# Kernel optimization log

Hardware: AMD Instinct MI355X
Metric: run time of the kernel (lower is better)

Reference implementation:

```python
import jax, jax.numpy as jnp
import numpy as np
import math

B, N, D, H, DK, DI, L, C = 4, 512, 1024, 16, 64, 4096, 6, 16000
EPS = 1e-5


def pe_table(n, d):
    # faithful to PE() with d_inp == d_model == d
    pos = jnp.arange(n, dtype=jnp.float32)[:, None]
    div = jnp.exp(jnp.arange(0, d, 2, dtype=jnp.float32) * (-math.log(10000.0) / d))
    p = jnp.zeros((n, d), jnp.float32)
    p = p.at[:, 0::2].set(jnp.sin(pos * div))
    p = p.at[:, 1::2].set(jnp.cos(pos * div))
    return p[None]  # [1, n, d] broadcasts over batch (== torch repeat)


def layer_norm(x, g, b):
    mu = jnp.mean(x, -1, keepdims=True)
    var = jnp.mean(jnp.square(x - mu), -1, keepdims=True)
    return (x - mu) / jnp.sqrt(var + EPS) * g + b


def mha(q_in, k_in, v_in, Wq, Wk, Wv, Wo, mask):
    # Wq/Wk/Wv: [H, D, DK]; batched equivalent of the per-head Linear loop
    q = jnp.einsum('bnd,hdk->bhnk', q_in, Wq)
    k = jnp.einsum('bmd,hdk->bhmk', k_in, Wk)
    v = jnp.einsum('bmd,hdk->bhmk', v_in, Wv)
    s = jnp.einsum('bhnk,bhmk->bhnm', q, k) / math.sqrt(q.shape[-1])
    s = jnp.where(mask[:, None] == 0, -jnp.inf, s)
    a = jax.nn.softmax(s, -1)
    o = jnp.einsum('bhnm,bhmk->bhnk', a, v)
    b_, h, n, dv = o.shape
    # concat heads in order (dim=-1) then Wo
    return o.transpose(0, 2, 1, 3).reshape(b_, n, h * dv) @ Wo


def ffn(x, W1, b1, W2, b2):
    return jax.nn.relu(x @ W1 + b1) @ W2 + b2


def transformer_fwd(encoder_input, decoder_input, encoder_mask, decoder_mask,
                    enc_Wq, enc_Wk, enc_Wv, enc_Wo, enc_W1, enc_b1, enc_W2, enc_b2,
                    enc_g1, enc_beta1, enc_g2, enc_beta2,
                    dec_sWq, dec_sWk, dec_sWv, dec_sWo, dec_cWq, dec_cWk, dec_cWv, dec_cWo,
                    dec_W1, dec_b1, dec_W2, dec_b2,
                    dec_g1, dec_beta1, dec_g2, dec_beta2, dec_g3, dec_beta3,
                    pred_W, pred_b):
    n, d = encoder_input.shape[1], encoder_input.shape[2]
    pe = pe_table(n, d)

    def enc_step(x, p):
        Wq, Wk, Wv, Wo, W1, b1, W2, b2, g1, bb1, g2, bb2 = p
        h1 = layer_norm(x + mha(x, x, x, Wq, Wk, Wv, Wo, encoder_mask), g1, bb1)
        return layer_norm(h1 + ffn(h1, W1, b1, W2, b2), g2, bb2), None

    enc_out, _ = jax.lax.scan(
        enc_step, encoder_input + pe,
        (enc_Wq, enc_Wk, enc_Wv, enc_Wo, enc_W1, enc_b1, enc_W2, enc_b2,
         enc_g1, enc_beta1, enc_g2, enc_beta2))

    # decoder uses encoder_mask[:, :t, :] with t == n (full mask here)
    def dec_step(x, p):
        (sWq, sWk, sWv, sWo, cWq, cWk, cWv, cWo,
         W1, b1, W2, b2, g1, bb1, g2, bb2, g3, bb3) = p
        h1 = layer_norm(x + mha(x, x, x, sWq, sWk, sWv, sWo, decoder_mask), g1, bb1)
        h2 = layer_norm(h1 + mha(h1, enc_out, enc_out, cWq, cWk, cWv, cWo, encoder_mask), g2, bb2)
        return layer_norm(h2 + ffn(h2, W1, b1, W2, b2), g3, bb3), None

    dec_out, _ = jax.lax.scan(
        dec_step, decoder_input + pe,
        (dec_sWq, dec_sWk, dec_sWv, dec_sWo, dec_cWq, dec_cWk, dec_cWv, dec_cWo,
         dec_W1, dec_b1, dec_W2, dec_b2,
         dec_g1, dec_beta1, dec_g2, dec_beta2, dec_g3, dec_beta3))

    return jax.nn.softmax(dec_out @ pred_W + pred_b, -1)


def setup_inputs():
    key = jax.random.key(0)
    ks = iter(jax.random.split(key, 32))
    w = lambda *s: jax.random.normal(next(ks), s, jnp.float32) * 0.02
    return {
        'encoder_input': jax.random.normal(next(ks), (B, N, D), jnp.float32),
        'decoder_input': jax.random.normal(next(ks), (B, N, D), jnp.float32),
        'encoder_mask': jnp.ones((B, N, N), jnp.int32),
        'decoder_mask': jnp.tril(jnp.ones((B, N, N), jnp.int32)),  # causal, as Mask()
        'enc_Wq': w(L, H, D, DK), 'enc_Wk': w(L, H, D, DK), 'enc_Wv': w(L, H, D, DK),
        'enc_Wo': w(L, H * DK, D),
        'enc_W1': w(L, D, DI), 'enc_b1': jnp.zeros((L, DI), jnp.float32),
        'enc_W2': w(L, DI, D), 'enc_b2': jnp.zeros((L, D), jnp.float32),
        'enc_g1': jnp.ones((L, D), jnp.float32), 'enc_beta1': jnp.zeros((L, D), jnp.float32),
        'enc_g2': jnp.ones((L, D), jnp.float32), 'enc_beta2': jnp.zeros((L, D), jnp.float32),
        'dec_sWq': w(L, H, D, DK), 'dec_sWk': w(L, H, D, DK), 'dec_sWv': w(L, H, D, DK),
        'dec_sWo': w(L, H * DK, D),
        'dec_cWq': w(L, H, D, DK), 'dec_cWk': w(L, H, D, DK), 'dec_cWv': w(L, H, D, DK),
        'dec_cWo': w(L, H * DK, D),
        'dec_W1': w(L, D, DI), 'dec_b1': jnp.zeros((L, DI), jnp.float32),
        'dec_W2': w(L, DI, D), 'dec_b2': jnp.zeros((L, D), jnp.float32),
        'dec_g1': jnp.ones((L, D), jnp.float32), 'dec_beta1': jnp.zeros((L, D), jnp.float32),
        'dec_g2': jnp.ones((L, D), jnp.float32), 'dec_beta2': jnp.zeros((L, D), jnp.float32),
        'dec_g3': jnp.ones((L, D), jnp.float32), 'dec_beta3': jnp.zeros((L, D), jnp.float32),
        'pred_W': w(D, C), 'pred_b': jnp.zeros((C,), jnp.float32),
    }


def reference(encoder_input, decoder_input, encoder_mask, decoder_mask,
              enc_Wq, enc_Wk, enc_Wv, enc_Wo, enc_W1, enc_b1, enc_W2, enc_b2,
              enc_g1, enc_beta1, enc_g2, enc_beta2,
              dec_sWq, dec_sWk, dec_sWv, dec_sWo, dec_cWq, dec_cWk, dec_cWv, dec_cWo,
              dec_W1, dec_b1, dec_W2, dec_b2,
              dec_g1, dec_beta1, dec_g2, dec_beta2, dec_g3, dec_beta3,
              pred_W, pred_b):
    return transformer_fwd(encoder_input, decoder_input, encoder_mask, decoder_mask,
                           enc_Wq, enc_Wk, enc_Wv, enc_Wo, enc_W1, enc_b1, enc_W2, enc_b2,
                           enc_g1, enc_beta1, enc_g2, enc_beta2,
                           dec_sWq, dec_sWk, dec_sWv, dec_sWo, dec_cWq, dec_cWk, dec_cWv, dec_cWo,
                           dec_W1, dec_b1, dec_W2, dec_b2,
                           dec_g1, dec_beta1, dec_g2, dec_beta2, dec_g3, dec_beta3,
                           pred_W, pred_b)
```

## Files before the change

kernel.cpp:

```cpp
#include <hip/hip_runtime.h>
#include <hip/hip_bf16.h>
#include <cstdint>

using bf16 = __hip_bfloat16;
typedef __attribute__((ext_vector_type(8))) short short8;
typedef __attribute__((ext_vector_type(4))) float floatx4;

constexpr int B_ = 4, N_ = 512, D_ = 1024, H_ = 16, DK_ = 64, DI_ = 4096, L_ = 6, C_ = 16000;
constexpr int M_ = B_ * N_;
constexpr int HK_ = H_ * DK_;

#define GLL16(gp, lp)                                                                         \
    __builtin_amdgcn_global_load_lds((const __attribute__((address_space(1))) void*)(gp),     \
                                     (__attribute__((address_space(3))) void*)(lp), 16, 0, 0)

template<int OUTB, int BIAS, int RELU>
__global__ __launch_bounds__(256)
void gemm_bt(const bf16* __restrict__ Ag, const bf16* __restrict__ Bg,
             void* __restrict__ Cg, const float* __restrict__ bias,
             int Mdim, int Ndim, int Kdim, int lda, int ldb, int ldc,
             int nbH, int gm, long sAb, long sAh, long sBb, long sBh, long sCb, long sCh)
{
    __shared__ bf16 As[128 * 32];
    __shared__ bf16 Bs[128 * 32];

    const int gx = gridDim.x, gy = gridDim.y;
    const int Sz = gx * gy;
    const int nwg = Sz * (int)gridDim.z;
    const int lin = ((int)blockIdx.z * gy + (int)blockIdx.y) * gx + (int)blockIdx.x;
    const int xcd = lin & 7, idx = lin >> 3;
    const int q = nwg >> 3, r = nwg & 7;
    const int w = (xcd < r ? xcd * (q + 1) : r * (q + 1) + (xcd - r) * q) + idx;
    const int bz = w / Sz;
    const int u = w - bz * Sz;
    const int gw = gm * gx;
    const int grp = u / gw;
    const int rem = u - grp * gw;
    const int gm0 = grp * gm;
    const int gsz = min(gm, gy - gm0);
    const int mt = gm0 + rem % gsz;
    const int nt = rem / gsz;
    const int m0 = mt * 128;
    const int n0 = nt * 128;

    const int bb = bz / nbH;
    const int hh = bz - bb * nbH;
    Ag += (long)bb * sAb + (long)hh * sAh;
    Bg += (long)bb * sBb + (long)hh * sBh;
    const long coff = (long)bb * sCb + (long)hh * sCh;

    const int t = threadIdx.x;
    const int lane = t & 63;
    const int wid = t >> 6;
    const int wm = wid & 1, wn = wid >> 1;

    const int sRow = t >> 2;
    const int sColE = (t & 3) * 8;
    const int ar0 = min(m0 + sRow, Mdim - 1);
    const int ar1 = min(m0 + 64 + sRow, Mdim - 1);
    const int br0 = min(n0 + sRow, Ndim - 1);
    const int br1 = min(n0 + 64 + sRow, Ndim - 1);
    const bf16* pa0 = Ag + (long)ar0 * lda + sColE;
    const bf16* pa1 = Ag + (long)ar1 * lda + sColE;
    const bf16* pb0 = Bg + (long)br0 * ldb + sColE;
    const bf16* pb1 = Bg + (long)br1 * ldb + sColE;
    bf16* la0 = As + sRow * 32 + sColE;
    bf16* la1 = As + (64 + sRow) * 32 + sColE;
    bf16* lb0 = Bs + sRow * 32 + sColE;
    bf16* lb1 = Bs + (64 + sRow) * 32 + sColE;

    floatx4 acc[4][4] = {};
    const int fm = lane & 15;
    const int fk = (lane >> 4) * 8;

    for (int k0 = 0; k0 < Kdim; k0 += 32) {
        __syncthreads();
        GLL16(pa0 + k0, la0);
        GLL16(pa1 + k0, la1);
        GLL16(pb0 + k0, lb0);
        GLL16(pb1 + k0, lb1);
        __syncthreads();

        short8 af[4], bfr[4];
        #pragma unroll
        for (int i = 0; i < 4; ++i)
            af[i] = *(const short8*)(As + (wm * 64 + i * 16 + fm) * 32 + fk);
        #pragma unroll
        for (int j = 0; j < 4; ++j)
            bfr[j] = *(const short8*)(Bs + (wn * 64 + j * 16 + fm) * 32 + fk);
        #pragma unroll
        for (int i = 0; i < 4; ++i)
            #pragma unroll
            for (int j = 0; j < 4; ++j)
                acc[i][j] = __builtin_amdgcn_mfma_f32_16x16x32_bf16(af[i], bfr[j], acc[i][j], 0, 0, 0);
    }

    const int rb = (lane >> 4) * 4;
    #pragma unroll
    for (int j = 0; j < 4; ++j) {
        int c = n0 + wn * 64 + j * 16 + fm;
        if (c >= Ndim) continue;
        float bv = BIAS ? bias[c] : 0.f;
        #pragma unroll
        for (int i = 0; i < 4; ++i) {
            #pragma unroll
            for (int r2 = 0; r2 < 4; ++r2) {
                int row = m0 + wm * 64 + i * 16 + rb + r2;
                if (row >= Mdim) continue;
                float v = acc[i][j][r2] + bv;
                if (RELU) v = fmaxf(v, 0.f);
                long cidx = coff + (long)row * ldc + c;
                if (OUTB) ((bf16*)Cg)[cidx] = __float2bfloat16(v);
                else      ((float*)Cg)[cidx] = v;
            }
        }
    }
}

__global__ __launch_bounds__(256)
void transpose_cvt(const float* __restrict__ src, bf16* __restrict__ dst,
                   int Zi, int R, int C,
                   long sSrcZo, long sSrcZi, long sDstZo, long sDstZi, int dstLD)
{
    __shared__ float tile[32][33];
    const int z = blockIdx.z;
    const int zo = z / Zi, zi = z - zo * Zi;
    const float* s = src + (long)zo * sSrcZo + (long)zi * sSrcZi;
    bf16* d = dst + (long)zo * sDstZo + (long)zi * sDstZi;
    const int c0 = blockIdx.x * 32, r0 = blockIdx.y * 32;
    const int tx = threadIdx.x, ty = threadIdx.y;
    #pragma unroll
    for (int k = 0; k < 4; ++k)
        tile[ty + 8 * k][tx] = s[(long)(r0 + ty + 8 * k) * C + (c0 + tx)];
    __syncthreads();
    #pragma unroll
    for (int k = 0; k < 4; ++k) {
        int cc = ty + 8 * k;
        d[(long)(c0 + cc) * dstLD + (r0 + tx)] = __float2bfloat16(tile[tx][cc]);
    }
}

__device__ __forceinline__ float wave_max(float v) {
    #pragma unroll
    for (int o = 32; o > 0; o >>= 1) v = fmaxf(v, __shfl_down(v, o, 64));
    return v;
}
__device__ __forceinline__ float wave_sum(float v) {
    #pragma unroll
    for (int o = 32; o > 0; o >>= 1) v += __shfl_down(v, o, 64);
    return v;
}

__global__ __launch_bounds__(256)
void add_pe(const float* __restrict__ in, float* __restrict__ outf, bf16* __restrict__ outb)
{
    const long i = (long)blockIdx.x * 256 + threadIdx.x;
    const int d = (int)(i & (D_ - 1));
    const int n = (int)((i >> 10) & (N_ - 1));
    const float div = __expf((float)(d & ~1) * (-9.2103403719761836f / (float)D_));
    const float ang = (float)n * div;
    const float pe = (d & 1) ? cosf(ang) : sinf(ang);
    const float v = in[i] + pe;
    outf[i] = v;
    outb[i] = __float2bfloat16(v);
}

template<int CAUSAL>
__global__ __launch_bounds__(256)
void attn_softmax(const float* __restrict__ S, bf16* __restrict__ P)
{
    const int row = blockIdx.x, bh = blockIdx.y;
    const long base = ((long)bh * N_ + row) * N_;
    const int t = threadIdx.x, lane = t & 63, w = t >> 6;
    const int valid = CAUSAL ? row + 1 : N_;
    float v0 = (t < valid) ? S[base + t] * 0.125f : -__builtin_inff();
    float v1 = (t + 256 < valid) ? S[base + t + 256] * 0.125f : -__builtin_inff();
    __shared__ float r1[4], r2[4];
    float m = wave_max(fmaxf(v0, v1));
    if (lane == 0) r1[w] = m;
    __syncthreads();
    const float mx = fmaxf(fmaxf(r1[0], r1[1]), fmaxf(r1[2], r1[3]));
    const float e0 = __expf(v0 - mx);
    const float e1 = __expf(v1 - mx);
    float s = wave_sum(e0 + e1);
    if (lane == 0) r2[w] = s;
    __syncthreads();
    const float inv = 1.f / ((r2[0] + r2[1]) + (r2[2] + r2[3]));
    P[base + t] = __float2bfloat16(e0 * inv);
    P[base + t + 256] = __float2bfloat16(e1 * inv);
}

struct bf16x4 { bf16 a, b, c, d; };

__global__ __launch_bounds__(256)
void add_ln(const float* __restrict__ X, const float* __restrict__ Y,
            const float* __restrict__ g, const float* __restrict__ be,
            float* __restrict__ outf, bf16* __restrict__ outb)
{
    const int row = blockIdx.x;
    const long base = (long)row * D_;
    const int t = threadIdx.x, lane = t & 63, w = t >> 6;
    const float4 xv = ((const float4*)(X + base))[t];
    const float4 yv = ((const float4*)(Y + base))[t];
    const float a0 = xv.x + yv.x, a1 = xv.y + yv.y, a2 = xv.z + yv.z, a3 = xv.w + yv.w;
    float s = a0 + a1 + a2 + a3;
    float qq = a0 * a0 + a1 * a1 + a2 * a2 + a3 * a3;
    #pragma unroll
    for (int o = 32; o > 0; o >>= 1) { s += __shfl_down(s, o, 64); qq += __shfl_down(qq, o, 64); }
    __shared__ float rs[4], rq[4];
    if (lane == 0) { rs[w] = s; rq[w] = qq; }
    __syncthreads();
    const float S = (rs[0] + rs[1]) + (rs[2] + rs[3]);
    const float Q = (rq[0] + rq[1]) + (rq[2] + rq[3]);
    const float mu = S * (1.f / (float)D_);
    const float var = Q * (1.f / (float)D_) - mu * mu;
    const float rstd = rsqrtf(var + 1e-5f);
    const float4 gv = ((const float4*)g)[t];
    const float4 bv = ((const float4*)be)[t];
    const float o0 = (a0 - mu) * rstd * gv.x + bv.x;
    const float o1 = (a1 - mu) * rstd * gv.y + bv.y;
    const float o2 = (a2 - mu) * rstd * gv.z + bv.z;
    const float o3 = (a3 - mu) * rstd * gv.w + bv.w;
    ((float4*)(outf + base))[t] = make_float4(o0, o1, o2, o3);
    bf16x4 pk{__float2bfloat16(o0), __float2bfloat16(o1), __float2bfloat16(o2), __float2bfloat16(o3)};
    ((bf16x4*)(outb + base))[t] = pk;
}

__global__ __launch_bounds__(256)
void softmax_C(float* __restrict__ X)
{
    constexpr int NI = 63;
    const int row = blockIdx.x;
    float* x = X + (long)row * C_;
    const int t = threadIdx.x, lane = t & 63, w = t >> 6;
    float v[NI];
    float m = -__builtin_inff();
    #pragma unroll
    for (int i = 0; i < NI; ++i) {
        int c = t + i * 256;
        v[i] = (c < C_) ? x[c] : -__builtin_inff();
        m = fmaxf(m, v[i]);
    }
    __shared__ float r1[4], r2[4];
    m = wave_max(m);
    if (lane == 0) r1[w] = m;
    __syncthreads();
    const float mx = fmaxf(fmaxf(r1[0], r1[1]), fmaxf(r1[2], r1[3]));
    float s = 0.f;
    #pragma unroll
    for (int i = 0; i < NI; ++i) { v[i] = __expf(v[i] - mx); s += v[i]; }
    s = wave_sum(s);
    if (lane == 0) r2[w] = s;
    __syncthreads();
    const float inv = 1.f / ((r2[0] + r2[1]) + (r2[2] + r2[3]));
    #pragma unroll
    for (int i = 0; i < NI; ++i) {
        int c = t + i * 256;
        if (c < C_) x[c] = v[i] * inv;
    }
}

static inline int cdiv(int a, int b) { return (a + b - 1) / b; }

static void launch_gemm(hipStream_t st, int outb, int bias_en, int relu,
                        const bf16* A, const bf16* Bm, void* C, const float* bias,
                        int M, int N, int K, int lda, int ldb, int ldc,
                        int nbB = 1, int nbH = 1,
                        long sAb = 0, long sAh = 0, long sBb = 0, long sBh = 0,
                        long sCb = 0, long sCh = 0)
{
    const int gmx = cdiv(N, 128), gmy = cdiv(M, 128);
    const int nwg = gmx * gmy * nbB * nbH;
    const int per = nwg > 8 ? nwg / 8 : 1;
    int gm = 1;
    while (gm * gm < per && gm < gmy) ++gm;
    dim3 g(gmx, gmy, nbB * nbH);
    dim3 b(256);
    if (outb) {
        if (relu) gemm_bt<1,1,1><<<g,b,0,st>>>(A,Bm,C,bias,M,N,K,lda,ldb,ldc,nbH,gm,sAb,sAh,sBb,sBh,sCb,sCh);
        else      gemm_bt<1,0,0><<<g,b,0,st>>>(A,Bm,C,bias,M,N,K,lda,ldb,ldc,nbH,gm,sAb,sAh,sBb,sBh,sCb,sCh);
    } else {
        if (bias_en) gemm_bt<0,1,0><<<g,b,0,st>>>(A,Bm,C,bias,M,N,K,lda,ldb,ldc,nbH,gm,sAb,sAh,sBb,sBh,sCb,sCh);
        else         gemm_bt<0,0,0><<<g,b,0,st>>>(A,Bm,C,bias,M,N,K,lda,ldb,ldc,nbH,gm,sAb,sAh,sBb,sBh,sCb,sCh);
    }
}

extern "C" void kernel_launch(void* const* d_in, const int* in_sizes, int n_in,
                              void* d_out, int out_size, void* d_ws, size_t ws_size,
                              hipStream_t stream)
{
    (void)in_sizes; (void)n_in; (void)out_size; (void)ws_size;

    const float* enc_in  = (const float*)d_in[0];
    const float* dec_in  = (const float*)d_in[1];
    const float* enc_Wq  = (const float*)d_in[4];
    const float* enc_Wk  = (const float*)d_in[5];
    const float* enc_Wv  = (const float*)d_in[6];
    const float* enc_Wo  = (const float*)d_in[7];
    const float* enc_W1  = (const float*)d_in[8];
    const float* enc_b1  = (const float*)d_in[9];
    const float* enc_W2  = (const float*)d_in[10];
    const float* enc_b2  = (const float*)d_in[11];
    const float* enc_g1  = (const float*)d_in[12];
    const float* enc_be1 = (const float*)d_in[13];
    const float* enc_g2  = (const float*)d_in[14];
    const float* enc_be2 = (const float*)d_in[15];
    const float* dec_sWq = (const float*)d_in[16];
    const float* dec_sWk = (const float*)d_in[17];
    const float* dec_sWv = (const float*)d_in[18];
    const float* dec_sWo = (const float*)d_in[19];
    const float* dec_cWq = (const float*)d_in[20];
    const float* dec_cWk = (const float*)d_in[21];
    const float* dec_cWv = (const float*)d_in[22];
    const float* dec_cWo = (const float*)d_in[23];
    const float* dec_W1  = (const float*)d_in[24];
    const float* dec_b1  = (const float*)d_in[25];
    const float* dec_W2  = (const float*)d_in[26];
    const float* dec_b2  = (const float*)d_in[27];
    const float* dec_g1  = (const float*)d_in[28];
    const float* dec_be1 = (const float*)d_in[29];
    const float* dec_g2  = (const float*)d_in[30];
    const float* dec_be2 = (const float*)d_in[31];
    const float* dec_g3  = (const float*)d_in[32];
    const float* dec_be3 = (const float*)d_in[33];
    const float* pred_W  = (const float*)d_in[34];
    const float* pred_b  = (const float*)d_in[35];

    char* wsb = (char*)d_ws;
    size_t off = 0;
    auto alloc = [&](size_t bytes) -> void* {
        void* p = wsb + off;
        off += (bytes + 255) & ~(size_t)255;
        return p;
    };

    bf16* encWqkT  = (bf16*)alloc((size_t)L_ * 2 * HK_ * D_ * 2);
    bf16* encWvT   = (bf16*)alloc((size_t)L_ * HK_ * D_ * 2);
    bf16* encWoT   = (bf16*)alloc((size_t)L_ * D_ * HK_ * 2);
    bf16* encW1T   = (bf16*)alloc((size_t)L_ * DI_ * D_ * 2);
    bf16* encW2T   = (bf16*)alloc((size_t)L_ * D_ * DI_ * 2);
    bf16* decSWqkT = (bf16*)alloc((size_t)L_ * 2 * HK_ * D_ * 2);
    bf16* decSWvT  = (bf16*)alloc((size_t)L_ * HK_ * D_ * 2);
    bf16* decSWoT  = (bf16*)alloc((size_t)L_ * D_ * HK_ * 2);
    bf16* decCWqkT = (bf16*)alloc((size_t)L_ * 2 * HK_ * D_ * 2);
    bf16* decCWvT  = (bf16*)alloc((size_t)L_ * HK_ * D_ * 2);
    bf16* decCWoT  = (bf16*)alloc((size_t)L_ * D_ * HK_ * 2);
    bf16* decW1T   = (bf16*)alloc((size_t)L_ * DI_ * D_ * 2);
    bf16* decW2T   = (bf16*)alloc((size_t)L_ * D_ * DI_ * 2);
    bf16* predWT   = (bf16*)alloc((size_t)C_ * D_ * 2);
    float* xf   = (float*)alloc((size_t)M_ * D_ * 4);
    bf16*  xb   = (bf16*) alloc((size_t)M_ * D_ * 2);
    float* dxf  = (float*)alloc((size_t)M_ * D_ * 4);
    bf16*  dxb  = (bf16*) alloc((size_t)M_ * D_ * 2);
    float* h1f  = (float*)alloc((size_t)M_ * D_ * 4);
    bf16*  h1b  = (bf16*) alloc((size_t)M_ * D_ * 2);
    float* h2f  = (float*)alloc((size_t)M_ * D_ * 4);
    bf16*  h2b  = (bf16*) alloc((size_t)M_ * D_ * 2);
    float* tmpf = (float*)alloc((size_t)M_ * D_ * 4);
    bf16*  qkb  = (bf16*) alloc((size_t)M_ * 2 * HK_ * 2);
    bf16*  vtb  = (bf16*) alloc((size_t)HK_ * M_ * 2);
    float* Sb   = (float*)alloc((size_t)B_ * H_ * N_ * N_ * 4);
    bf16*  Pb   = (bf16*) alloc((size_t)B_ * H_ * N_ * N_ * 2);
    bf16*  ob   = (bf16*) alloc((size_t)M_ * HK_ * 2);
    bf16*  hg   = (bf16*) alloc((size_t)M_ * DI_ * 2);

    auto tr = [&](const float* src, bf16* dst, int Zo, int Zi, int R, int C,
                  long sSrcZo, long sSrcZi, long sDstZo, long sDstZi, int dstLD) {
        dim3 g(C / 32, R / 32, Zo * Zi);
        dim3 b(32, 8);
        transpose_cvt<<<g, b, 0, stream>>>(src, dst, Zi, R, C, sSrcZo, sSrcZi, sDstZo, sDstZi, dstLD);
    };
    const long sA_src_o = (long)H_ * D_ * DK_, sA_src_i = (long)D_ * DK_;
    const long sA_dst_i = (long)DK_ * D_;
    tr(enc_Wq,  encWqkT,                     L_, H_, D_, DK_, sA_src_o, sA_src_i, (long)2*HK_*D_, sA_dst_i, D_);
    tr(enc_Wk,  encWqkT + (size_t)HK_*D_,    L_, H_, D_, DK_, sA_src_o, sA_src_i, (long)2*HK_*D_, sA_dst_i, D_);
    tr(enc_Wv,  encWvT,                      L_, H_, D_, DK_, sA_src_o, sA_src_i, (long)HK_*D_,   sA_dst_i, D_);
    tr(enc_Wo,  encWoT,  L_, 1, HK_, D_,  (long)HK_*D_, 0, (long)D_*HK_, 0, HK_);
    tr(enc_W1,  encW1T,  L_, 1, D_, DI_,  (long)D_*DI_, 0, (long)DI_*D_, 0, D_);
    tr(enc_W2,  encW2T,  L_, 1, DI_, D_,  (long)DI_*D_, 0, (long)D_*DI_, 0, DI_);
    tr(dec_sWq, decSWqkT,                    L_, H_, D_, DK_, sA_src_o, sA_src_i, (long)2*HK_*D_, sA_dst_i, D_);
    tr(dec_sWk, decSWqkT + (size_t)HK_*D_,   L_, H_, D_, DK_, sA_src_o, sA_src_i, (long)2*HK_*D_, sA_dst_i, D_);
    tr(dec_sWv, decSWvT,                     L_, H_, D_, DK_, sA_src_o, sA_src_i, (long)HK_*D_,   sA_dst_i, D_);
    tr(dec_sWo, decSWoT, L_, 1, HK_, D_,  (long)HK_*D_, 0, (long)D_*HK_, 0, HK_);
    tr(dec_cWq, decCWqkT,                    L_, H_, D_, DK_, sA_src_o, sA_src_i, (long)2*HK_*D_, sA_dst_i, D_);
    tr(dec_cWk, decCWqkT + (size_t)HK_*D_,   L_, H_, D_, DK_, sA_src_o, sA_src_i, (long)2*HK_*D_, sA_dst_i, D_);
    tr(dec_cWv, decCWvT,                     L_, H_, D_, DK_, sA_src_o, sA_src_i, (long)HK_*D_,   sA_dst_i, D_);
    tr(dec_cWo, decCWoT, L_, 1, HK_, D_,  (long)HK_*D_, 0, (long)D_*HK_, 0, HK_);
    tr(dec_W1,  decW1T,  L_, 1, D_, DI_,  (long)D_*DI_, 0, (long)DI_*D_, 0, D_);
    tr(dec_W2,  decW2T,  L_, 1, DI_, D_,  (long)DI_*D_, 0, (long)D_*DI_, 0, DI_);
    tr(pred_W,  predWT,  1,  1, D_, C_,   0, 0, 0, 0, D_);

    add_pe<<<(M_ * D_) / 256, 256, 0, stream>>>(enc_in, xf, xb);
    add_pe<<<(M_ * D_) / 256, 256, 0, stream>>>(dec_in, dxf, dxb);

    auto attention = [&](const bf16* qin, const bf16* kvin,
                         const bf16* wqk, const bf16* wv, const bf16* wo, bool causal) {
        if (qin == kvin) {
            launch_gemm(stream, 1,0,0, qin, wqk, qkb, nullptr, M_, 2*HK_, D_, D_, D_, 2*HK_);
        } else {
            launch_gemm(stream, 1,0,0, qin,  wqk,                  qkb,       nullptr, M_, HK_, D_, D_, D_, 2*HK_);
            launch_gemm(stream, 1,0,0, kvin, wqk + (size_t)HK_*D_, qkb + HK_, nullptr, M_, HK_, D_, D_, D_, 2*HK_);
        }
        launch_gemm(stream, 1,0,0, wv, kvin, vtb, nullptr, HK_, M_, D_, D_, D_, M_);
        launch_gemm(stream, 0,0,0, qkb, qkb + HK_, Sb, nullptr,
                    N_, N_, DK_, 2*HK_, 2*HK_, N_,
                    B_, H_,
                    (long)N_*2*HK_, (long)DK_,
                    (long)N_*2*HK_, (long)DK_,
                    (long)H_*N_*N_, (long)N_*N_);
        dim3 sg(N_, B_ * H_);
        if (causal) attn_softmax<1><<<sg, 256, 0, stream>>>(Sb, Pb);
        else        attn_softmax<0><<<sg, 256, 0, stream>>>(Sb, Pb);
        launch_gemm(stream, 1,0,0, Pb, vtb, ob, nullptr,
                    N_, DK_, N_, N_, M_, HK_,
                    B_, H_,
                    (long)H_*N_*N_, (long)N_*N_,
                    (long)N_,       (long)DK_*M_,
                    (long)N_*HK_,   (long)DK_);
        launch_gemm(stream, 0,0,0, ob, wo, tmpf, nullptr, M_, D_, HK_, HK_, HK_, D_);
    };

    for (int l = 0; l < L_; ++l) {
        const bf16* wqk = encWqkT + (size_t)l * 2 * HK_ * D_;
        const bf16* wv  = encWvT  + (size_t)l * HK_ * D_;
        const bf16* wo  = encWoT  + (size_t)l * D_ * HK_;
        const bf16* w1  = encW1T  + (size_t)l * DI_ * D_;
        const bf16* w2  = encW2T  + (size_t)l * D_ * DI_;
        attention(xb, xb, wqk, wv, wo, false);
        add_ln<<<M_, 256, 0, stream>>>(xf, tmpf, enc_g1 + l*D_, enc_be1 + l*D_, h1f, h1b);
        launch_gemm(stream, 1,1,1, h1b, w1, hg, enc_b1 + l*DI_, M_, DI_, D_, D_, D_, DI_);
        launch_gemm(stream, 0,1,0, hg, w2, tmpf, enc_b2 + l*D_, M_, D_, DI_, DI_, DI_, D_);
        add_ln<<<M_, 256, 0, stream>>>(h1f, tmpf, enc_g2 + l*D_, enc_be2 + l*D_, xf, xb);
    }

    for (int l = 0; l < L_; ++l) {
        const bf16* swqk = decSWqkT + (size_t)l * 2 * HK_ * D_;
        const bf16* swv  = decSWvT  + (size_t)l * HK_ * D_;
        const bf16* swo  = decSWoT  + (size_t)l * D_ * HK_;
        const bf16* cwqk = decCWqkT + (size_t)l * 2 * HK_ * D_;
        const bf16* cwv  = decCWvT  + (size_t)l * HK_ * D_;
        const bf16* cwo  = decCWoT  + (size_t)l * D_ * HK_;
        const bf16* w1   = decW1T   + (size_t)l * DI_ * D_;
        const bf16* w2   = decW2T   + (size_t)l * D_ * DI_;
        attention(dxb, dxb, swqk, swv, swo, true);
        add_ln<<<M_, 256, 0, stream>>>(dxf, tmpf, dec_g1 + l*D_, dec_be1 + l*D_, h1f, h1b);
        attention(h1b, xb, cwqk, cwv, cwo, false);
        add_ln<<<M_, 256, 0, stream>>>(h1f, tmpf, dec_g2 + l*D_, dec_be2 + l*D_, h2f, h2b);
        launch_gemm(stream, 1,1,1, h2b, w1, hg, dec_b1 + l*DI_, M_, DI_, D_, D_, D_, DI_);
        launch_gemm(stream, 0,1,0, hg, w2, tmpf, dec_b2 + l*D_, M_, D_, DI_, DI_, DI_, D_);
        add_ln<<<M_, 256, 0, stream>>>(h2f, tmpf, dec_g3 + l*D_, dec_be3 + l*D_, dxf, dxb);
    }

    launch_gemm(stream, 0,1,0, dxb, predWT, d_out, pred_b, M_, C_, D_, D_, D_, C_);
    softmax_C<<<M_, 256, 0, stream>>>((float*)d_out);
}
```

Measured before the change: 5.902 ms.

## Double-buffer GEMM LDS tiles with async global-to-LDS prefetch

Doubles the LDS A/B tile buffers in the bf16 GEMM and prefetches the next K-slice with global_load_lds while the current slice is consumed by MFMAs. Explicit vmcnt waits and raw barriers replace the two __syncthreads per iteration. The goal is to hide global memory latency behind compute. In exchange, LDS use per block doubles, which may lower occupancy, and the hand-written waitcnt logic is fragile.

```diff
diff --git a/kernel.cpp b/kernel.cpp
--- a/kernel.cpp
+++ b/kernel.cpp
@@ -13,6 +13,10 @@
 #define GLL16(gp, lp)                                                                         \
     __builtin_amdgcn_global_load_lds((const __attribute__((address_space(1))) void*)(gp),     \
                                      (__attribute__((address_space(3))) void*)(lp), 16, 0, 0)
+
+#define WAITV4 asm volatile("s_waitcnt vmcnt(4)" ::: "memory")
+#define WAITV0 asm volatile("s_waitcnt vmcnt(0)" ::: "memory")
+#define BAR    do { asm volatile("" ::: "memory"); __builtin_amdgcn_s_barrier(); asm volatile("" ::: "memory"); } while (0)
 
 template<int OUTB, int BIAS, int RELU>
 __global__ __launch_bounds__(256)
@@ -21,8 +25,8 @@
              int Mdim, int Ndim, int Kdim, int lda, int ldb, int ldc,
              int nbH, int gm, long sAb, long sAh, long sBb, long sBh, long sCb, long sCh)
 {
-    __shared__ bf16 As[128 * 32];
-    __shared__ bf16 Bs[128 * 32];
+    __shared__ bf16 As[2 * 128 * 32];
+    __shared__ bf16 Bs[2 * 128 * 32];
 
     const int gx = gridDim.x, gy = gridDim.y;
     const int Sz = gx * gy;
@@ -39,9 +43,9 @@
     const int gm0 = grp * gm;
     const int gsz = min(gm, gy - gm0);
     const int mt = gm0 + rem % gsz;
-    const int nt = rem / gsz;
+    const int nt2 = rem / gsz;
     const int m0 = mt * 128;
-    const int n0 = nt * 128;
+    const int n0 = nt2 * 128;
 
     const int bb = bz / nbH;
     const int hh = bz - bb * nbH;
@@ -64,35 +68,46 @@
     const bf16* pa1 = Ag + (long)ar1 * lda + sColE;
     const bf16* pb0 = Bg + (long)br0 * ldb + sColE;
     const bf16* pb1 = Bg + (long)br1 * ldb + sColE;
-    bf16* la0 = As + sRow * 32 + sColE;
-    bf16* la1 = As + (64 + sRow) * 32 + sColE;
-    bf16* lb0 = Bs + sRow * 32 + sColE;
-    bf16* lb1 = Bs + (64 + sRow) * 32 + sColE;
+    const int ldsOff = sRow * 32 + sColE;
 
     floatx4 acc[4][4] = {};
     const int fm = lane & 15;
     const int fk = (lane >> 4) * 8;
 
-    for (int k0 = 0; k0 < Kdim; k0 += 32) {
-        __syncthreads();
-        GLL16(pa0 + k0, la0);
-        GLL16(pa1 + k0, la1);
-        GLL16(pb0 + k0, lb0);
-        GLL16(pb1 + k0, lb1);
-        __syncthreads();
-
+    auto stage = [&](int k, bf16* aB, bf16* bB) {
+        GLL16(pa0 + k, aB + ldsOff);
+        GLL16(pa1 + k, aB + 64 * 32 + ldsOff);
+        GLL16(pb0 + k, bB + ldsOff);
+        GLL16(pb1 + k, bB + 64 * 32 + ldsOff);
+    };
+    auto compute = [&](const bf16* aB, const bf16* bB) {
         short8 af[4], bfr[4];
         #pragma unroll
         for (int i = 0; i < 4; ++i)
-            af[i] = *(const short8*)(As + (wm * 64 + i * 16 + fm) * 32 + fk);
+            af[i] = *(const short8*)(aB + (wm * 64 + i * 16 + fm) * 32 + fk);
         #pragma unroll
         for (int j = 0; j < 4; ++j)
-            bfr[j] = *(const short8*)(Bs + (wn * 64 + j * 16 + fm) * 32 + fk);
+            bfr[j] = *(const short8*)(bB + (wn * 64 + j * 16 + fm) * 32 + fk);
         #pragma unroll
         for (int i = 0; i < 4; ++i)
             #pragma unroll
             for (int j = 0; j < 4; ++j)
                 acc[i][j] = __builtin_amdgcn_mfma_f32_16x16x32_bf16(af[i], bfr[j], acc[i][j], 0, 0, 0);
+    };
+
+    const int nt = Kdim >> 5;
+    stage(0, As, Bs);
+    for (int k0 = 0; k0 < nt; k0 += 2) {
+        if (k0 + 1 < nt) { stage((k0 + 1) << 5, As + 4096, Bs + 4096); WAITV4; } else { WAITV0; }
+        BAR;
+        compute(As, Bs);
+        BAR;
+        if (k0 + 1 < nt) {
+            if (k0 + 2 < nt) { stage((k0 + 2) << 5, As, Bs); WAITV4; } else { WAITV0; }
+            BAR;
+            compute(As + 4096, Bs + 4096);
+            BAR;
+        }
     }
 
     const int rb = (lane >> 4) * 4;
```

After: 5.858 ms. Within noise of the previous version (-0.7%).
